# Optimization experiments

Hardware: AMD Instinct MI355X
Metric: run time of the kernel (lower is better)

## Reference

```python
import jax, jax.numpy as jnp
import numpy as np

B, D, K = 131072, 64, 4096

def setup_inputs() -> dict:
    key = jax.random.key(0)
    k1, k2 = jax.random.split(key)
    z_e = jax.random.normal(k1, (B, D), dtype=jnp.float32)
    # nn.init.uniform_(-1/K, 1/K)
    codebook = jax.random.uniform(k2, (K, D), dtype=jnp.float32, minval=-1.0 / K, maxval=1.0 / K)
    return {"z_e": z_e, "codebook": codebook}

def reference(z_e, codebook):
    # squared-distance expansion: ||z||^2 + ||e||^2 - 2 z.e  -> (B, K)
    z2 = jnp.sum(z_e * z_e, axis=1, keepdims=True)          # (B, 1)
    e2 = jnp.sum(codebook * codebook, axis=1)[None, :]       # (1, K)
    ze = jnp.einsum('bd,kd->bk', z_e, codebook)              # (B, K)
    dist = z2 + e2 - 2.0 * ze
    codes = jnp.argmin(dist, axis=1)                         # (B,) int
    z_q = codebook[codes]                                    # (B, D) gather
    return (z_q, codes)
```

## Files before the change

kernel.cpp:

```cpp
#include <hip/hip_runtime.h>
#include <math.h>

#define Bn 131072
#define Dn 64
#define Kn 4096
#define TK 64
#define NKT (Kn / TK)

typedef _Float16 f16x8 __attribute__((ext_vector_type(8)));
typedef float f32x4 __attribute__((ext_vector_type(4)));

__device__ __forceinline__ unsigned umn(unsigned a, unsigned b) { return a < b ? a : b; }
__device__ __forceinline__ unsigned umx(unsigned a, unsigned b) { return a > b ? a : b; }

__global__ __launch_bounds__(512, 4) void vq_main(const float* __restrict__ z,
                                                  const float* __restrict__ cb,
                                                  float* __restrict__ out) {
  __shared__ __align__(16) unsigned char smem[34816];
  unsigned char* tb0 = smem;
  unsigned char* tb1 = smem + 8192;
  const int tid = threadIdx.x;
  const int lane = tid & 63;
  const int w = tid >> 6;
  const int q = lane >> 4;
  const int col = lane & 15;
  const int row0 = blockIdx.x * 256;

  f16x8 A[2][2];
#pragma unroll
  for (int i = 0; i < 2; ++i)
#pragma unroll
    for (int c = 0; c < 2; ++c) {
      const float* zp = z + (size_t)(row0 + w * 32 + i * 16 + col) * Dn + c * 32 + q * 8;
      float4 x0 = *(const float4*)zp;
      float4 x1 = *(const float4*)(zp + 4);
      f16x8 a;
      a[0] = (_Float16)(-2.f * x0.x); a[1] = (_Float16)(-2.f * x0.y);
      a[2] = (_Float16)(-2.f * x0.z); a[3] = (_Float16)(-2.f * x0.w);
      a[4] = (_Float16)(-2.f * x1.x); a[5] = (_Float16)(-2.f * x1.y);
      a[6] = (_Float16)(-2.f * x1.z); a[7] = (_Float16)(-2.f * x1.w);
      A[i][c] = a;
    }

  const int n = tid >> 3;
  const int p = tid & 7;
  const int wr = n * 128 + ((p ^ (n & 7)) << 4);

  f32x4 acc[2][4];
  unsigned k1[2][4], k2[2][4];
#pragma unroll
  for (int i = 0; i < 2; ++i)
#pragma unroll
    for (int r = 0; r < 4; ++r) { k1[i][r] = 0xFFFFFFFFu; k2[i][r] = 0xFFFFFFFFu; }
  unsigned tg[4] = {0u, 1u, 2u, 3u};
  const f32x4 c256 = {256.f, 256.f, 256.f, 256.f};

  float4 pf0, pf1;
  {
    const float4* g = (const float4*)(cb + (size_t)n * Dn + p * 8);
    float4 c0 = g[0], c1 = g[1];
    f16x8 h;
    h[0] = (_Float16)(c0.x * 4096.f); h[1] = (_Float16)(c0.y * 4096.f);
    h[2] = (_Float16)(c0.z * 4096.f); h[3] = (_Float16)(c0.w * 4096.f);
    h[4] = (_Float16)(c1.x * 4096.f); h[5] = (_Float16)(c1.y * 4096.f);
    h[6] = (_Float16)(c1.z * 4096.f); h[7] = (_Float16)(c1.w * 4096.f);
    *(f16x8*)(tb0 + wr) = h;
    const float4* g1 = (const float4*)(cb + (size_t)(TK + n) * Dn + p * 8);
    pf0 = g1[0]; pf1 = g1[1];
  }
  __syncthreads();

  for (int kt = 0; kt < NKT; ++kt) {
    unsigned char* tcur = (kt & 1) ? tb1 : tb0;
    unsigned char* tnxt = (kt & 1) ? tb0 : tb1;
    if (kt + 1 < NKT) {
      f16x8 h;
      h[0] = (_Float16)(pf0.x * 4096.f); h[1] = (_Float16)(pf0.y * 4096.f);
      h[2] = (_Float16)(pf0.z * 4096.f); h[3] = (_Float16)(pf0.w * 4096.f);
      h[4] = (_Float16)(pf1.x * 4096.f); h[5] = (_Float16)(pf1.y * 4096.f);
      h[6] = (_Float16)(pf1.z * 4096.f); h[7] = (_Float16)(pf1.w * 4096.f);
      *(f16x8*)(tnxt + wr) = h;
    }
    if (kt + 2 < NKT) {
      const float4* g = (const float4*)(cb + ((size_t)(kt + 2) * TK + n) * Dn + p * 8);
      pf0 = g[0]; pf1 = g[1];
    }

#pragma unroll
    for (int c = 0; c < 2; ++c)
#pragma unroll
      for (int t = 0; t < 4; ++t) {
        f16x8 Bf = *(const f16x8*)(tcur + (t * 16 + col) * 128 + (((c * 4 + q) ^ (col & 7)) << 4));
#pragma unroll
        for (int i = 0; i < 2; ++i)
          acc[i][t] = __builtin_amdgcn_mfma_f32_16x16x32_f16(A[i][c], Bf,
                                                             (c == 0) ? c256 : acc[i][t], 0, 0, 0);
      }

#pragma unroll
    for (int i = 0; i < 2; ++i)
#pragma unroll
      for (int r = 0; r < 4; ++r) {
        unsigned K0 = (__float_as_uint(acc[i][0][r]) & 0xFFFFFF00u) | tg[0];
        unsigned K1v = (__float_as_uint(acc[i][1][r]) & 0xFFFFFF00u) | tg[1];
        unsigned K2v = (__float_as_uint(acc[i][2][r]) & 0xFFFFFF00u) | tg[2];
        unsigned K3v = (__float_as_uint(acc[i][3][r]) & 0xFFFFFF00u) | tg[3];
        unsigned lo = umn(K0, K1v), hi = umx(K0, K1v);
        k2[i][r] = umn(umn(k2[i][r], umx(k1[i][r], lo)), hi);
        k1[i][r] = umn(k1[i][r], lo);
        lo = umn(K2v, K3v); hi = umx(K2v, K3v);
        k2[i][r] = umn(umn(k2[i][r], umx(k1[i][r], lo)), hi);
        k1[i][r] = umn(k1[i][r], lo);
      }
#pragma unroll
    for (int t = 0; t < 4; ++t) tg[t] += 4;

    __syncthreads();
  }

  unsigned* dmp = (unsigned*)smem;
#pragma unroll
  for (int i = 0; i < 2; ++i)
#pragma unroll
    for (int r = 0; r < 4; ++r) {
      int rr = i * 16 + q * 4 + r;
      int rb = w * 32 + rr;
      dmp[rb * 33 + col * 2] = k1[i][r];
      dmp[rb * 33 + col * 2 + 1] = k2[i][r];
    }
  __syncthreads();

  {
    const int rl = tid >> 1;
    const int half = tid & 1;
    const unsigned* keys = dmp + rl * 33 + half * 16;
    unsigned mk = 0xFFFFFFFFu;
    for (int j = 0; j < 16; ++j) mk = umn(mk, keys[j]);
    const float lim = __uint_as_float(mk & 0xFFFFFF00u) + 0.5f;

    const float4* zr4 = (const float4*)(z + (size_t)(row0 + rl) * Dn);

    float r8[8];
#pragma unroll
    for (int g = 0; g < 2; ++g) {
      float4 v = zr4[g]; int j = g * 4;
      r8[j + 0] = __fmul_rn(v.x, v.x); r8[j + 1] = __fmul_rn(v.y, v.y);
      r8[j + 2] = __fmul_rn(v.z, v.z); r8[j + 3] = __fmul_rn(v.w, v.w);
    }
#pragma unroll
    for (int g = 2; g < 16; ++g) {
      float4 v = zr4[g]; int j = (g & 1) * 4;
      r8[j + 0] = __fadd_rn(r8[j + 0], __fmul_rn(v.x, v.x));
      r8[j + 1] = __fadd_rn(r8[j + 1], __fmul_rn(v.y, v.y));
      r8[j + 2] = __fadd_rn(r8[j + 2], __fmul_rn(v.z, v.z));
      r8[j + 3] = __fadd_rn(r8[j + 3], __fmul_rn(v.w, v.w));
    }
    float z2f = __fadd_rn(__fadd_rn(__fadd_rn(r8[0], r8[1]), __fadd_rn(r8[2], r8[3])),
                          __fadd_rn(__fadd_rn(r8[4], r8[5]), __fadd_rn(r8[6], r8[7])));

    float bq = INFINITY; int bc = Kn;
    for (int j = 0; j < 16; ++j) {
      unsigned key = keys[j];
      float sc = __uint_as_float(key & 0xFFFFFF00u);
      if (sc > lim) continue;
      int cnd = half * 16 + j;
      int tag = (int)(key & 0xFFu);
      int code = (tag >> 2) * 64 + (tag & 3) * 16 + (cnd >> 1);
      const float4* cr = (const float4*)(cb + (size_t)code * Dn);
      double ze = 0.0;
      float e8[8];
#pragma unroll
      for (int g = 0; g < 16; ++g) {
        float4 ev = cr[g]; float4 zv = zr4[g];
        ze += (double)ev.x * (double)zv.x + (double)ev.y * (double)zv.y +
              (double)ev.z * (double)zv.z + (double)ev.w * (double)zv.w;
        int jj = (g & 1) * 4;
        if (g < 2) {
          e8[jj + 0] = __fmul_rn(ev.x, ev.x); e8[jj + 1] = __fmul_rn(ev.y, ev.y);
          e8[jj + 2] = __fmul_rn(ev.z, ev.z); e8[jj + 3] = __fmul_rn(ev.w, ev.w);
        } else {
          e8[jj + 0] = __fadd_rn(e8[jj + 0], __fmul_rn(ev.x, ev.x));
          e8[jj + 1] = __fadd_rn(e8[jj + 1], __fmul_rn(ev.y, ev.y));
          e8[jj + 2] = __fadd_rn(e8[jj + 2], __fmul_rn(ev.z, ev.z));
          e8[jj + 3] = __fadd_rn(e8[jj + 3], __fmul_rn(ev.w, ev.w));
        }
      }
      float e2f = __fadd_rn(__fadd_rn(__fadd_rn(e8[0], e8[1]), __fadd_rn(e8[2], e8[3])),
                            __fadd_rn(__fadd_rn(e8[4], e8[5]), __fadd_rn(e8[6], e8[7])));
      float zef = (float)ze;
      float t1 = __fadd_rn(z2f, e2f);
      float t2 = __fmul_rn(2.0f, zef);
      float qv = __fadd_rn(t1, -t2);
      if (qv < bq || (qv == bq && code < bc)) { bq = qv; bc = code; }
    }
    float obq = __shfl_xor(bq, 1);
    int obc = __shfl_xor(bc, 1);
    if (obq < bq || (obq == bq && obc < bc)) { bq = obq; bc = obc; }
    if (half == 0) {
      ((int*)(smem + 33792))[rl] = bc;
      out[(size_t)Bn * Dn + row0 + rl] = (float)bc;
    }
  }
  __syncthreads();

  {
    const float4* cb4 = (const float4*)cb;
    float4* out4 = (float4*)out;
    const int* wc = (const int*)(smem + 33792);
#pragma unroll
    for (int i = 0; i < 8; ++i) {
      int t = i * 512 + tid;
      int r = t >> 4, c2 = t & 15;
      int wn = wc[r];
      out4[(size_t)(row0 + r) * 16 + c2] = cb4[(size_t)wn * 16 + c2];
    }
  }
}

extern "C" void kernel_launch(void* const* d_in, const int* in_sizes, int n_in,
                              void* d_out, int out_size, void* d_ws, size_t ws_size,
                              hipStream_t stream) {
  const float* z = (const float*)d_in[0];
  const float* cb = (const float*)d_in[1];
  float* out = (float*)d_out;
  vq_main<<<Bn / 256, 512, 0, stream>>>(z, cb, out);
}
```

Measured before the change: 220.6 us.

## Precompute fp16 swizzled codebook image and stream tiles via global_load_lds

Adds a pre-pass kernel that converts the codebook to scaled fp16 once, in the swizzled LDS tile layout, and writes it to workspace. The main kernel then copies each tile straight into LDS with direct global-to-LDS loads, using manual vmcnt waits and raw barriers in place of per-block register prefetch, conversion and ds_write. The top-2 update is also rewritten with v_med3_u32 to cut min/max operations. The cost is an extra kernel launch and reliance on hand-placed waitcnt and barrier ordering being correct.

```diff
diff --git a/kernel.cpp b/kernel.cpp
--- a/kernel.cpp
+++ b/kernel.cpp
@@ -1,5 +1,6 @@
 #include <hip/hip_runtime.h>
 #include <math.h>
+#include <stdint.h>
 
 #define Bn 131072
 #define Dn 64
@@ -12,9 +13,41 @@
 
 __device__ __forceinline__ unsigned umn(unsigned a, unsigned b) { return a < b ? a : b; }
 __device__ __forceinline__ unsigned umx(unsigned a, unsigned b) { return a > b ? a : b; }
+__device__ __forceinline__ unsigned umed3(unsigned a, unsigned b, unsigned c) {
+  unsigned d;
+  asm("v_med3_u32 %0, %1, %2, %3" : "=v"(d) : "v"(a), "v"(b), "v"(c));
+  return d;
+}
+__device__ __forceinline__ unsigned umn3(unsigned a, unsigned b, unsigned c) {
+  return umn(umn(a, b), c);
+}
+
+__device__ __forceinline__ void stage16(const void* g, void* l) {
+  __builtin_amdgcn_global_load_lds((const __attribute__((address_space(1))) unsigned int*)g,
+                                   (__attribute__((address_space(3))) unsigned int*)l,
+                                   16, 0, 0);
+}
+
+__global__ __launch_bounds__(256) void cvt_cb(const float* __restrict__ cb,
+                                              unsigned char* __restrict__ img) {
+  int u = blockIdx.x * 256 + threadIdx.x;
+  int g = u >> 3;
+  int p = u & 7;
+  int kt = g >> 6;
+  int n = g & 63;
+  const float4* s = (const float4*)(cb + (size_t)g * Dn + p * 8);
+  float4 c0 = s[0], c1 = s[1];
+  f16x8 h;
+  h[0] = (_Float16)(c0.x * 4096.f); h[1] = (_Float16)(c0.y * 4096.f);
+  h[2] = (_Float16)(c0.z * 4096.f); h[3] = (_Float16)(c0.w * 4096.f);
+  h[4] = (_Float16)(c1.x * 4096.f); h[5] = (_Float16)(c1.y * 4096.f);
+  h[6] = (_Float16)(c1.z * 4096.f); h[7] = (_Float16)(c1.w * 4096.f);
+  *(f16x8*)(img + (size_t)kt * 8192 + n * 128 + ((p ^ (n & 7)) << 4)) = h;
+}
 
 __global__ __launch_bounds__(512, 4) void vq_main(const float* __restrict__ z,
                                                   const float* __restrict__ cb,
+                                                  const unsigned char* __restrict__ img,
                                                   float* __restrict__ out) {
   __shared__ __align__(16) unsigned char smem[34816];
   unsigned char* tb0 = smem;
@@ -26,6 +59,9 @@
   const int col = lane & 15;
   const int row0 = blockIdx.x * 256;
 
+  const unsigned char* wsrc = img + tid * 16;
+  stage16(wsrc, tb0 + tid * 16);
+
   f16x8 A[2][2];
 #pragma unroll
   for (int i = 0; i < 2; ++i)
@@ -42,10 +78,6 @@
       A[i][c] = a;
     }
 
-  const int n = tid >> 3;
-  const int p = tid & 7;
-  const int wr = n * 128 + ((p ^ (n & 7)) << 4);
-
   f32x4 acc[2][4];
   unsigned k1[2][4], k2[2][4];
 #pragma unroll
@@ -54,37 +86,18 @@
     for (int r = 0; r < 4; ++r) { k1[i][r] = 0xFFFFFFFFu; k2[i][r] = 0xFFFFFFFFu; }
   unsigned tg[4] = {0u, 1u, 2u, 3u};
   const f32x4 c256 = {256.f, 256.f, 256.f, 256.f};
-
-  float4 pf0, pf1;
-  {
-    const float4* g = (const float4*)(cb + (size_t)n * Dn + p * 8);
-    float4 c0 = g[0], c1 = g[1];
-    f16x8 h;
-    h[0] = (_Float16)(c0.x * 4096.f); h[1] = (_Float16)(c0.y * 4096.f);
-    h[2] = (_Float16)(c0.z * 4096.f); h[3] = (_Float16)(c0.w * 4096.f);
-    h[4] = (_Float16)(c1.x * 4096.f); h[5] = (_Float16)(c1.y * 4096.f);
-    h[6] = (_Float16)(c1.z * 4096.f); h[7] = (_Float16)(c1.w * 4096.f);
-    *(f16x8*)(tb0 + wr) = h;
-    const float4* g1 = (const float4*)(cb + (size_t)(TK + n) * Dn + p * 8);
-    pf0 = g1[0]; pf1 = g1[1];
-  }
-  __syncthreads();
 
   for (int kt = 0; kt < NKT; ++kt) {
     unsigned char* tcur = (kt & 1) ? tb1 : tb0;
     unsigned char* tnxt = (kt & 1) ? tb0 : tb1;
     if (kt + 1 < NKT) {
-      f16x8 h;
-      h[0] = (_Float16)(pf0.x * 4096.f); h[1] = (_Float16)(pf0.y * 4096.f);
-      h[2] = (_Float16)(pf0.z * 4096.f); h[3] = (_Float16)(pf0.w * 4096.f);
-      h[4] = (_Float16)(pf1.x * 4096.f); h[5] = (_Float16)(pf1.y * 4096.f);
-      h[6] = (_Float16)(pf1.z * 4096.f); h[7] = (_Float16)(pf1.w * 4096.f);
-      *(f16x8*)(tnxt + wr) = h;
-    }
-    if (kt + 2 < NKT) {
-      const float4* g = (const float4*)(cb + ((size_t)(kt + 2) * TK + n) * Dn + p * 8);
-      pf0 = g[0]; pf1 = g[1];
-    }
+      stage16(wsrc + (size_t)(kt + 1) * 8192, tnxt + tid * 16);
+      asm volatile("s_waitcnt vmcnt(1)" ::: "memory");
+    } else {
+      asm volatile("s_waitcnt vmcnt(0)" ::: "memory");
+    }
+    __builtin_amdgcn_s_barrier();
+    __builtin_amdgcn_sched_barrier(0);
 
 #pragma unroll
     for (int c = 0; c < 2; ++c)
@@ -105,19 +118,20 @@
         unsigned K1v = (__float_as_uint(acc[i][1][r]) & 0xFFFFFF00u) | tg[1];
         unsigned K2v = (__float_as_uint(acc[i][2][r]) & 0xFFFFFF00u) | tg[2];
         unsigned K3v = (__float_as_uint(acc[i][3][r]) & 0xFFFFFF00u) | tg[3];
-        unsigned lo = umn(K0, K1v), hi = umx(K0, K1v);
-        k2[i][r] = umn(umn(k2[i][r], umx(k1[i][r], lo)), hi);
-        k1[i][r] = umn(k1[i][r], lo);
-        lo = umn(K2v, K3v); hi = umx(K2v, K3v);
-        k2[i][r] = umn(umn(k2[i][r], umx(k1[i][r], lo)), hi);
-        k1[i][r] = umn(k1[i][r], lo);
+        unsigned s1 = umn(K0, K1v), s2 = umx(K0, K1v);
+        unsigned s3 = umn(K2v, K3v), s4 = umx(K2v, K3v);
+        unsigned m3 = umed3(k1[i][r], s1, s3);
+        unsigned n3 = umn3(k2[i][r], s2, s4);
+        k1[i][r] = umn3(k1[i][r], s1, s3);
+        k2[i][r] = umn(m3, n3);
       }
 #pragma unroll
     for (int t = 0; t < 4; ++t) tg[t] += 4;
 
-    __syncthreads();
+    __builtin_amdgcn_s_barrier();
   }
 
+  __syncthreads();
   unsigned* dmp = (unsigned*)smem;
 #pragma unroll
   for (int i = 0; i < 2; ++i)
@@ -223,5 +237,7 @@
   const float* z = (const float*)d_in[0];
   const float* cb = (const float*)d_in[1];
   float* out = (float*)d_out;
-  vq_main<<<Bn / 256, 512, 0, stream>>>(z, cb, out);
-}
+  unsigned char* img = (unsigned char*)d_ws;
+  cvt_cb<<<128, 256, 0, stream>>>(cb, img);
+  vq_main<<<Bn / 256, 512, 0, stream>>>(z, cb, img, out);
+}
```

After: 193.0 us. -12.5%, faster.
